# Performance work log

Measured on AMD Instinct MI355X. Metric: run time of the kernel, lower is better.

## Reference

```python
import jax, jax.numpy as jnp
import numpy as np

M, U, H, C, EMB, HID = 4096, 8, 8, 64, 64, 128
N = M * U            # 32768 nodes
E = 131072           # edges
D = H * C            # 512 = heads * hidden_channels
NUM_LAYERS = 4
IN0 = 6              # 2 coords + mask + speed + cost + arrival
SCALE = np.float32(1.0 / np.sqrt(C))

def _lin(x, W, b):
    return x @ W + b

def _transformer_conv(x, src, dst, Wq, bq, Wk, bk, Wv, bv, Ws, bs):
    # PyG TransformerConv: x_j = x[src], x_i = x[dst]; softmax over edges per dst
    n = x.shape[0]
    q = _lin(x, Wq, bq).reshape(n, H, C)
    k = _lin(x, Wk, bk).reshape(n, H, C)
    v = _lin(x, Wv, bv).reshape(n, H, C)
    alpha = jnp.einsum('ehc,ehc->eh', q[dst], k[src]) * SCALE   # [E,H]
    amax = jax.ops.segment_max(alpha, dst, num_segments=n)       # [N,H]
    ex = jnp.exp(alpha - amax[dst])
    denom = jax.ops.segment_sum(ex, dst, num_segments=n)         # [N,H]
    agg = jax.ops.segment_sum(ex[:, :, None] * v[src], dst, num_segments=n)  # [N,H,C]
    out = agg / (denom[:, :, None] + 1e-16)
    return out.reshape(n, D) + _lin(x, Ws, bs)                   # concat heads + root skip

def _forward(mission_coords, uavs_info, speeds, cost_matrix, arrival_times,
             Wq0, bq0, Wk0, bk0, Wv0, bv0, Ws0, bs0,
             Wq, bq, Wk, bk, Wv, bv, Ws, bs,
             fc_W, fc_b, aW1, ab1, aW2, ab2, cW1, cb1, cW2, cb2,
             edge_index, batch, action_mask):
    mc = jnp.broadcast_to(mission_coords[:, None, :], (M, U, 2))
    mk = jnp.broadcast_to(action_mask[:, None, None].astype(jnp.float32), (M, U, 1))
    sp = jnp.broadcast_to(speeds[None, :, None], (M, U, 1))
    cm = cost_matrix.T[:, :, None]
    at = arrival_times.T[:, :, None]
    x = jnp.concatenate([mc, mk, sp, cm, at], axis=-1).reshape(N, IN0)
    src, dst = edge_index[0], edge_index[1]
    x = jax.nn.relu(_transformer_conv(x, src, dst, Wq0, bq0, Wk0, bk0, Wv0, bv0, Ws0, bs0))
    for l in range(NUM_LAYERS - 1):
        x = jax.nn.relu(_transformer_conv(x, src, dst, Wq[l], bq[l], Wk[l], bk[l], Wv[l], bv[l], Ws[l], bs[l]))
    new_batch = jnp.repeat(batch, U)                             # [N]
    sums = jax.ops.segment_sum(x, new_batch, num_segments=1)
    cnts = jax.ops.segment_sum(jnp.ones((N,), x.dtype), new_batch, num_segments=1)
    pooled = sums / cnts[:, None]                                # [1, D]
    emb = _lin(pooled, fc_W, fc_b)                               # [1, EMB]
    emb_exp = jnp.tile(emb, (U, 1))                              # [U, EMB]
    combined = jnp.concatenate([uavs_info, emb_exp, speeds[:, None]], axis=-1)  # [U, EMB+3]
    action_probs = jax.nn.softmax(_lin(jax.nn.relu(_lin(combined, aW1, ab1)), aW2, ab2), axis=-1)
    state_values = _lin(jax.nn.relu(_lin(combined, cW1, cb1)), cW2, cb2)
    return action_probs, state_values

def setup_inputs() -> dict:
    key = jax.random.key(0)
    ks = jax.random.split(key, 40)
    def nrm(i, shape, s=0.05):
        return jax.random.normal(ks[i], shape, jnp.float32) * s
    z = lambda *s: jnp.zeros(s, jnp.float32)
    L = NUM_LAYERS - 1
    inp = dict(
        mission_coords=jax.random.uniform(ks[0], (M, 2), jnp.float32),
        uavs_info=nrm(1, (U, 2), 1.0),
        speeds=jax.random.uniform(ks[2], (U,), jnp.float32) + 0.5,
        cost_matrix=jax.random.uniform(ks[3], (U, M), jnp.float32),
        arrival_times=jax.random.uniform(ks[4], (U, M), jnp.float32),
        edge_index=jax.random.randint(ks[5], (2, E), 0, N),
        batch=jnp.zeros((M,), jnp.int32),
        action_mask=jax.random.randint(ks[6], (M,), 0, 2),
        Wq0=nrm(7, (IN0, D)), bq0=z(D), Wk0=nrm(8, (IN0, D)), bk0=z(D),
        Wv0=nrm(9, (IN0, D)), bv0=z(D), Ws0=nrm(10, (IN0, D)), bs0=z(D),
        Wq=nrm(11, (L, D, D)), bq=z(L, D), Wk=nrm(12, (L, D, D)), bk=z(L, D),
        Wv=nrm(13, (L, D, D)), bv=z(L, D), Ws=nrm(14, (L, D, D)), bs=z(L, D),
        fc_W=nrm(15, (D, EMB)), fc_b=z(EMB),
        aW1=nrm(16, (EMB + 3, HID)), ab1=z(HID), aW2=nrm(17, (HID, M)), ab2=z(M),
        cW1=nrm(18, (EMB + 3, HID)), cb1=z(HID), cW2=nrm(19, (HID, 1)), cb2=z(1),
    )
    return inp

def reference(mission_coords, edge_index, batch, uavs_info, action_mask, speeds,
              cost_matrix, arrival_times,
              Wq0, bq0, Wk0, bk0, Wv0, bv0, Ws0, bs0,
              Wq, bq, Wk, bk, Wv, bv, Ws, bs,
              fc_W, fc_b, aW1, ab1, aW2, ab2, cW1, cb1, cW2, cb2):
    return _forward(mission_coords, uavs_info, speeds, cost_matrix, arrival_times,
                    Wq0, bq0, Wk0, bk0, Wv0, bv0, Ws0, bs0,
                    Wq, bq, Wk, bk, Wv, bv, Ws, bs,
                    fc_W, fc_b, aW1, ab1, aW2, ab2, cW1, cb1, cW2, cb2,
                    edge_index, batch, action_mask)
```

## Files before the change

kernel.cpp:

```cpp
#include <hip/hip_runtime.h>
#include <stdint.h>

typedef unsigned char u8;
typedef unsigned short u16;
typedef unsigned long long u64;
typedef __attribute__((ext_vector_type(8))) unsigned short u16x8;
typedef __attribute__((ext_vector_type(8))) __bf16 bf16x8;
typedef __attribute__((ext_vector_type(4))) float f32x4;
typedef __attribute__((ext_vector_type(2))) float f32x2;

#define NNODES 32768
#define NEDGES 131072
#define DDIM 512
#define QK4 2048
#define MM 4096
#define UU 8


__device__ __forceinline__ u16 f2bf(float f) {
    unsigned u = __builtin_bit_cast(unsigned, f);
    u += 0x7FFFu + ((u >> 16) & 1u);
    return (u16)(u >> 16);
}
__device__ __forceinline__ float bf2f(u16 h) {
    return __builtin_bit_cast(float, (unsigned)h << 16);
}
__device__ __forceinline__ void enc8(const float* f, int* lo, int* hi) {
    int a = __builtin_amdgcn_cvt_pk_fp8_f32(f[0], f[1], 0, false);
    a = __builtin_amdgcn_cvt_pk_fp8_f32(f[2], f[3], a, true);
    int b = __builtin_amdgcn_cvt_pk_fp8_f32(f[4], f[5], 0, false);
    b = __builtin_amdgcn_cvt_pk_fp8_f32(f[6], f[7], b, true);
    *lo = a;
    *hi = b;
}
__device__ __forceinline__ void dec8(int lo, int hi, float* f) {
    f32x2 a = __builtin_amdgcn_cvt_pk_f32_fp8(lo, false);
    f32x2 b = __builtin_amdgcn_cvt_pk_f32_fp8(lo, true);
    f32x2 c = __builtin_amdgcn_cvt_pk_f32_fp8(hi, false);
    f32x2 d = __builtin_amdgcn_cvt_pk_f32_fp8(hi, true);
    f[0] = a[0]; f[1] = a[1]; f[2] = b[0]; f[3] = b[1];
    f[4] = c[0]; f[5] = c[1]; f[6] = d[0]; f[7] = d[1];
}

__device__ __forceinline__ void load_lds16(const void* g, void* l) {
    __builtin_amdgcn_global_load_lds((__attribute__((address_space(1))) unsigned int*)(void*)g,
                                     (__attribute__((address_space(3))) unsigned int*)l, 16, 0, 0);
}

__global__ void k_prep(const float* __restrict__ mc, const int* __restrict__ mask,
                       const float* __restrict__ sp, const float* __restrict__ cm,
                       const float* __restrict__ at, float* __restrict__ x0,
                       const float* __restrict__ bq, const float* __restrict__ bk,
                       const float* __restrict__ bv, const float* __restrict__ bs,
                       float* __restrict__ bcat,
                       int* __restrict__ deg, float* __restrict__ pooled) {
    int b = blockIdx.x;
    int t = threadIdx.x;
    if (b < 128) {
        int node = b * 256 + t;
        deg[node] = 0;
        int m = node >> 3, u = node & 7;
        float* o = x0 + (size_t)node * 6;
        o[0] = mc[m * 2];
        o[1] = mc[m * 2 + 1];
        o[2] = (float)mask[m];
        o[3] = sp[u];
        o[4] = cm[u * MM + m];
        o[5] = at[u * MM + m];
    } else if (b < 152) {
        int i = (b - 128) * 256 + t;
        int n = i & (QK4 - 1);
        int l = i >> 11;
        int ty = n >> 9, nn = n & 511;
        const float* p = (ty == 0) ? bq : (ty == 1) ? bk : (ty == 2) ? bv : bs;
        bcat[(size_t)l * QK4 + n] = p[l * DDIM + nn];
    } else {
        pooled[(b - 152) * 256 + t] = 0.f;
    }
}

__global__ void k_c0(const float* __restrict__ Wq0, const float* __restrict__ bq0,
                     const float* __restrict__ Wk0, const float* __restrict__ bk0,
                     float* __restrict__ C0) {
    int i = threadIdx.x;
    if (i >= 392) return;
    int h = i / 49, r = i % 49;
    int d0 = h * 64;
    float s = 0.f;
    if (r < 36) {
        int a = r / 6, b = r % 6;
        for (int d = 0; d < 64; d++) s += Wq0[a * DDIM + d0 + d] * Wk0[b * DDIM + d0 + d];
    } else if (r < 42) {
        int a = r - 36;
        for (int d = 0; d < 64; d++) s += Wq0[a * DDIM + d0 + d] * bk0[d0 + d];
    } else if (r < 48) {
        int b = r - 42;
        for (int d = 0; d < 64; d++) s += Wk0[b * DDIM + d0 + d] * bq0[d0 + d];
    } else {
        for (int d = 0; d < 64; d++) s += bq0[d0 + d] * bk0[d0 + d];
    }
    C0[i] = s;
}

__global__ void k_wt(const float* __restrict__ Wq, const float* __restrict__ Wk,
                     const float* __restrict__ Wv, const float* __restrict__ Ws,
                     u16* __restrict__ Wt) {
    __shared__ float tile[32][33];
    int q = blockIdx.z;
    int l = q >> 2, t = q & 3;
    const float* src = ((t == 0) ? Wq : (t == 1) ? Wk : (t == 2) ? Wv : Ws) + (size_t)l * DDIM * DDIM;
    int k0 = blockIdx.x * 32, n0 = blockIdx.y * 32;
    int tx = threadIdx.x, ty = threadIdx.y;
#pragma unroll
    for (int r = 0; r < 4; r++) tile[ty + 8 * r][tx] = src[(size_t)(k0 + ty + 8 * r) * DDIM + n0 + tx];
    __syncthreads();
    u16* dst = Wt + (size_t)l * QK4 * DDIM + (size_t)t * DDIM * DDIM;
#pragma unroll
    for (int r = 0; r < 4; r++) {
        int n = n0 + ty + 8 * r;
        dst[(size_t)n * DDIM + k0 + tx] = f2bf(tile[tx][ty + 8 * r]);
    }
}

__global__ void k_count(const int* __restrict__ dst, int* __restrict__ deg) {
    int e = blockIdx.x * 256 + threadIdx.x;
    if (e < NEDGES) atomicAdd(&deg[dst[e]], 1);
}

__global__ __launch_bounds__(1024) void k_scan(const int* __restrict__ deg, int* __restrict__ offs,
                                               int* __restrict__ cursor) {
    __shared__ int sums[1024];
    int t = threadIdx.x;
    int base = t * 32;
    int local[32];
    int s = 0;
#pragma unroll
    for (int i = 0; i < 32; i++) { local[i] = s; s += deg[base + i]; }
    sums[t] = s;
    __syncthreads();
    for (int d = 1; d < 1024; d <<= 1) {
        int v = (t >= d) ? sums[t - d] : 0;
        __syncthreads();
        sums[t] += v;
        __syncthreads();
    }
    int excl = (t == 0) ? 0 : sums[t - 1];
#pragma unroll
    for (int i = 0; i < 32; i++) {
        int o = excl + local[i];
        offs[base + i] = o;
        cursor[base + i] = o;
    }
    if (t == 1023) offs[NNODES] = sums[1023];
}

__global__ void k_scatter(const int* __restrict__ src, const int* __restrict__ dst,
                          int* __restrict__ cursor, int* __restrict__ ssrc) {
    int e = blockIdx.x * 256 + threadIdx.x;
    if (e < NEDGES) {
        int pos = atomicAdd(&cursor[dst[e]], 1);
        ssrc[pos] = src[e];
    }
}

__global__ __launch_bounds__(256) void k_attn0(const float* __restrict__ x0, const float* __restrict__ C0,
                                               const float* __restrict__ Wv0, const float* __restrict__ bv0,
                                               const float* __restrict__ Ws0, const float* __restrict__ bs0,
                                               const int* __restrict__ offs, const int* __restrict__ ssrc,
                                               u16* __restrict__ Xout) {
    const int lane = threadIdx.x & 63;
    const int wv = threadIdx.x >> 6;
    const int h = lane & 7;
    float wV[8][6], wS[8][6], bV[8], bS[8];
#pragma unroll
    for (int j = 0; j < 8; ++j) {
        int c = lane + 64 * j;
        bV[j] = bv0[c];
        bS[j] = bs0[c];
#pragma unroll
        for (int a = 0; a < 6; ++a) {
            wV[j][a] = Wv0[a * DDIM + c];
            wS[j][a] = Ws0[a * DDIM + c];
        }
    }
    float Ah[36], uh[6], wh[6], ch;
#pragma unroll
    for (int r = 0; r < 36; ++r) Ah[r] = C0[h * 49 + r];
#pragma unroll
    for (int a = 0; a < 6; ++a) uh[a] = C0[h * 49 + 36 + a];
#pragma unroll
    for (int a = 0; a < 6; ++a) wh[a] = C0[h * 49 + 42 + a];
    ch = C0[h * 49 + 48];

    int node0 = (blockIdx.x * 4 + wv) * 8;
    for (int nn = 0; nn < 8; ++nn) {
        int node = node0 + nn;
        float xi[6];
#pragma unroll
        for (int a = 0; a < 6; ++a) xi[a] = x0[(size_t)node * 6 + a];
        float m = -INFINITY, l = 0.f;
        float xh[6];
#pragma unroll
        for (int a = 0; a < 6; ++a) xh[a] = 0.f;
        const int e0 = offs[node], e1 = offs[node + 1];
        for (int e = e0; e < e1; ++e) {
            int s = ssrc[e];
            float xj[6];
#pragma unroll
            for (int a = 0; a < 6; ++a) xj[a] = x0[(size_t)s * 6 + a];
            float alpha = ch;
#pragma unroll
            for (int a = 0; a < 6; ++a) {
                float t = uh[a];
#pragma unroll
                for (int b = 0; b < 6; ++b) t += Ah[a * 6 + b] * xj[b];
                alpha += xi[a] * t;
            }
#pragma unroll
            for (int b = 0; b < 6; ++b) alpha += wh[b] * xj[b];
            alpha *= 0.125f;
            float nm = fmaxf(m, alpha);
            float corr = __expf(m - nm);
            float p = __expf(alpha - nm);
            l = l * corr + p;
#pragma unroll
            for (int a = 0; a < 6; ++a) xh[a] = xh[a] * corr + p * xj[a];
            m = nm;
        }
#pragma unroll
        for (int j = 0; j < 8; ++j) {
            float lb = __shfl(l, j, 64);
            float num = lb * bV[j];
#pragma unroll
            for (int a = 0; a < 6; ++a) num += __shfl(xh[a], j, 64) * wV[j][a];
            float skip = bS[j];
#pragma unroll
            for (int a = 0; a < 6; ++a) skip += xi[a] * wS[j][a];
            float r = num / (lb + 1e-16f) + skip;
            Xout[(size_t)node * DDIM + lane + 64 * j] = f2bf(fmaxf(r, 0.f));
        }
    }
}

__global__ __launch_bounds__(256, 4) void k_gemm(const u16* __restrict__ X, const u16* __restrict__ Wt,
                                                 const float* __restrict__ bcat, u8* __restrict__ Q8,
                                                 u8* __restrict__ KV8, u16* __restrict__ S16) {
    __shared__ __align__(16) u16 smem[2 * 128 * 64];
    u16* As = smem;
    u16* Bs = smem + 128 * 64;
    const int tid = threadIdx.x;
    const int lane = tid & 63;
    const int w = tid >> 6;
    const int wm = w & 1, wn = w >> 1;
    const int bid = blockIdx.x;
    const int xcd = bid & 7;
    const int s = bid >> 3;
    const size_t arow0 = (size_t)(xcd * 32 + (s >> 4)) * 128;
    const size_t brow0 = (size_t)(s & 15) * 128;
    const int bt = (int)(brow0 >> 7);

    f32x4 acc[4][4];
#pragma unroll
    for (int i = 0; i < 4; i++)
#pragma unroll
        for (int j = 0; j < 4; j++) acc[i][j] = (f32x4){0.f, 0.f, 0.f, 0.f};

    const int la = lane & 7;
    const int quad = lane >> 4;
    const int lm = lane & 15;

    for (int kt = 0; kt < 8; ++kt) {
        const int k0 = kt * 64;
#pragma unroll
        for (int t = 0; t < 4; ++t) {
            int idx = (w * 4 + t) * 64 + lane;
            int m = idx >> 3;
            int c = la ^ (m & 7);
            const u16* ga = X + (arow0 + m) * DDIM + (k0 + c * 8);
            const u16* gb = Wt + (brow0 + m) * DDIM + (k0 + c * 8);
            load_lds16(ga, &As[(size_t)((w * 4 + t) * 64) * 8]);
            load_lds16(gb, &Bs[(size_t)((w * 4 + t) * 64) * 8]);
        }
        __syncthreads();
#pragma unroll
        for (int kk = 0; kk < 2; ++kk) {
            bf16x8 af[4], bfg[4];
            int c = kk * 4 + quad;
#pragma unroll
            for (int i = 0; i < 4; ++i) {
                int m = wm * 64 + i * 16 + lm;
                int slot = m * 8 + (c ^ (m & 7));
                af[i] = *(const bf16x8*)&As[(size_t)slot * 8];
            }
#pragma unroll
            for (int j = 0; j < 4; ++j) {
                int n = wn * 64 + j * 16 + lm;
                int slot = n * 8 + (c ^ (n & 7));
                bfg[j] = *(const bf16x8*)&Bs[(size_t)slot * 8];
            }
#pragma unroll
            for (int i = 0; i < 4; ++i)
#pragma unroll
                for (int j = 0; j < 4; ++j)
                    acc[i][j] = __builtin_amdgcn_mfma_f32_16x16x32_bf16(af[i], bfg[j], acc[i][j], 0, 0, 0);
        }
        __syncthreads();
    }

    float biasv[4];
#pragma unroll
    for (int j = 0; j < 4; ++j) biasv[j] = bcat[brow0 + wn * 64 + j * 16 + lm];

    u16* stg = smem;
    const int chunk = lane & 7;
    const int rrow = lane >> 3;
    const int colbase = (int)brow0 + wn * 64 + chunk * 8;
#pragma unroll
    for (int p = 0; p < 2; ++p) {
        __syncthreads();
#pragma unroll
        for (int ii = 0; ii < 2; ++ii) {
            int i = p * 2 + ii;
#pragma unroll
            for (int j = 0; j < 4; ++j) {
#pragma unroll
                for (int r = 0; r < 4; ++r) {
                    int lr = ii * 16 + quad * 4 + r;
                    int lc = j * 16 + lm;
                    stg[(size_t)(w * 32 + lr) * 72 + lc] = f2bf(acc[i][j][r] + biasv[j]);
                }
            }
        }
        __syncthreads();
#pragma unroll
        for (int it = 0; it < 4; ++it) {
            int row = it * 8 + rrow;
            u16x8 v = *(const u16x8*)&stg[(size_t)(w * 32 + row) * 72 + chunk * 8];
            size_t grow = arow0 + wm * 64 + p * 32 + row;
            if (bt < 4) {
                float f[8];
#pragma unroll
                for (int j = 0; j < 8; j++) f[j] = bf2f(v[j]);
                int lo, hi;
                enc8(f, &lo, &hi);
                *(int2*)(Q8 + grow * 512 + colbase) = make_int2(lo, hi);
            } else if (bt < 12) {
                float f[8];
#pragma unroll
                for (int j = 0; j < 8; j++) f[j] = bf2f(v[j]);
                int lo, hi;
                enc8(f, &lo, &hi);
                int kvcol = (bt < 8) ? (colbase - 512) : (colbase - 1024);
                int ofs = (bt < 8) ? 0 : 8;
                *(int2*)(KV8 + grow * 1024 + (size_t)(kvcol >> 3) * 16 + ofs) = make_int2(lo, hi);
            } else {
                *(u16x8*)(S16 + grow * 512 + (colbase - 1536)) = v;
            }
        }
    }
}

__global__ __launch_bounds__(256) void k_attn(const u8* __restrict__ Q8, const u8* __restrict__ KV8,
                                              const u16* __restrict__ S16, const int* __restrict__ offs,
                                              const int* __restrict__ ssrc, u16* __restrict__ Xout) {
    const int lane = threadIdx.x & 63;
    const int node = blockIdx.x * 4 + (threadIdx.x >> 6);
    const u64 q8 = *(const u64*)(Q8 + (size_t)node * 512 + (size_t)lane * 8);
    float qf[8];
    dec8((int)(q8 & 0xFFFFFFFFull), (int)(q8 >> 32), qf);
    float m = -INFINITY, l = 0.f;
    float acc[8];
#pragma unroll
    for (int j = 0; j < 8; j++) acc[j] = 0.f;
    const int e0 = offs[node], e1 = offs[node + 1];
    int e = e0;
    while (e < e1) {
        int nb = e1 - e;
        if (nb > 4) nb = 4;
        int4 kvb[4];
#pragma unroll
        for (int i = 0; i < 4; ++i) {
            if (i < nb) {
                int s = ssrc[e + i];
                kvb[i] = *(const int4*)(KV8 + (size_t)s * 1024 + (size_t)lane * 16);
            }
        }
#pragma unroll
        for (int i = 0; i < 4; ++i) {
            if (i >= nb) break;
            int4 kv = kvb[i];
            f32x2 k01 = __builtin_amdgcn_cvt_pk_f32_fp8(kv.x, false);
            f32x2 k23 = __builtin_amdgcn_cvt_pk_f32_fp8(kv.x, true);
            f32x2 k45 = __builtin_amdgcn_cvt_pk_f32_fp8(kv.y, false);
            f32x2 k67 = __builtin_amdgcn_cvt_pk_f32_fp8(kv.y, true);
            float d = qf[0] * k01[0] + qf[1] * k01[1] + qf[2] * k23[0] + qf[3] * k23[1] +
                      qf[4] * k45[0] + qf[5] * k45[1] + qf[6] * k67[0] + qf[7] * k67[1];
            d += __shfl_xor(d, 1, 64);
            d += __shfl_xor(d, 2, 64);
            d += __shfl_xor(d, 4, 64);
            float a = d * 0.125f;
            float nm = fmaxf(m, a);
            float corr = __expf(m - nm);
            float p = __expf(a - nm);
            l = l * corr + p;
            f32x2 v01 = __builtin_amdgcn_cvt_pk_f32_fp8(kv.z, false);
            f32x2 v23 = __builtin_amdgcn_cvt_pk_f32_fp8(kv.z, true);
            f32x2 v45 = __builtin_amdgcn_cvt_pk_f32_fp8(kv.w, false);
            f32x2 v67 = __builtin_amdgcn_cvt_pk_f32_fp8(kv.w, true);
            acc[0] = acc[0] * corr + p * v01[0];
            acc[1] = acc[1] * corr + p * v01[1];
            acc[2] = acc[2] * corr + p * v23[0];
            acc[3] = acc[3] * corr + p * v23[1];
            acc[4] = acc[4] * corr + p * v45[0];
            acc[5] = acc[5] * corr + p * v45[1];
            acc[6] = acc[6] * corr + p * v67[0];
            acc[7] = acc[7] * corr + p * v67[1];
            m = nm;
        }
        e += nb;
    }
    float inv = 1.0f / (l + 1e-16f);
    const u16x8 sv = *(const u16x8*)(S16 + (size_t)node * 512 + (size_t)lane * 8);
    u16x8 o;
#pragma unroll
    for (int j = 0; j < 8; j++) {
        float r = acc[j] * inv + bf2f(sv[j]);
        o[j] = f2bf(fmaxf(r, 0.f));
    }
    *(u16x8*)(Xout + (size_t)node * DDIM + (size_t)lane * 8) = o;
}

__global__ __launch_bounds__(256) void k_pool(const u16* __restrict__ X, float* __restrict__ pooled) {
    __shared__ float red[4][64][8];
    int t = threadIdx.x;
    int chunk = t & 63;
    int rofs = t >> 6;
    float s[8];
#pragma unroll
    for (int j = 0; j < 8; j++) s[j] = 0.f;
    int nd0 = blockIdx.x * 256;
    for (int nd = nd0 + rofs; nd < nd0 + 256; nd += 4) {
        u16x8 v = *(const u16x8*)&X[(size_t)nd * DDIM + chunk * 8];
#pragma unroll
        for (int j = 0; j < 8; j++) s[j] += bf2f(v[j]);
    }
#pragma unroll
    for (int j = 0; j < 8; j++) red[rofs][chunk][j] = s[j];
    __syncthreads();
    if (t < 64) {
#pragma unroll
        for (int j = 0; j < 8; j++) {
            float o = red[0][t][j] + red[1][t][j] + red[2][t][j] + red[3][t][j];
            atomicAdd(&pooled[t * 8 + j], o);
        }
    }
}

__global__ __launch_bounds__(1024) void k_heads(const float* __restrict__ pooled, const float* __restrict__ fcW,
                                                const float* __restrict__ fcb, const float* __restrict__ ui,
                                                const float* __restrict__ sp, const float* __restrict__ aW1,
                                                const float* __restrict__ ab1, const float* __restrict__ cW1,
                                                const float* __restrict__ cb1, const float* __restrict__ cW2,
                                                const float* __restrict__ cb2, float* __restrict__ hidden_a,
                                                float* __restrict__ out) {
    __shared__ float spool[512];
    __shared__ float semb[64];
    __shared__ float shc[8][128];
    int t = threadIdx.x;
    if (t < 512) spool[t] = pooled[t] * (1.0f / 32768.0f);
    __syncthreads();
    if (t < 64) {
        float s = fcb[t];
        for (int k = 0; k < 512; k++) s += spool[k] * fcW[k * 64 + t];
        semb[t] = s;
    }
    __syncthreads();
    int u = t >> 7, j = t & 127;
    float u0 = ui[u * 2], u1 = ui[u * 2 + 1], uspd = sp[u];
    float ha = ab1[j] + u0 * aW1[j] + u1 * aW1[128 + j] + uspd * aW1[66 * 128 + j];
    float hc = cb1[j] + u0 * cW1[j] + u1 * cW1[128 + j] + uspd * cW1[66 * 128 + j];
    for (int k = 0; k < 64; k++) {
        float e = semb[k];
        ha += e * aW1[(2 + k) * 128 + j];
        hc += e * cW1[(2 + k) * 128 + j];
    }
    ha = fmaxf(ha, 0.f);
    hc = fmaxf(hc, 0.f);
    hidden_a[u * 128 + j] = ha;
    shc[u][j] = hc;
    __syncthreads();
    if (t < 8) {
        float s = cb2[0];
        for (int k = 0; k < 128; k++) s += shc[t][k] * cW2[k];
        out[NNODES + t] = s;
    }
}

__global__ __launch_bounds__(1024) void k_actor(const float* __restrict__ hidden_a, const float* __restrict__ aW2,
                                                const float* __restrict__ ab2, float* __restrict__ out) {
    __shared__ float h[128];
    __shared__ float red[1024];
    int u = blockIdx.x, t = threadIdx.x;
    if (t < 128) h[t] = hidden_a[u * 128 + t];
    __syncthreads();
    float lg[4];
#pragma unroll
    for (int p = 0; p < 4; p++) {
        int mcol = t + p * 1024;
        float s = ab2[mcol];
        for (int k = 0; k < 128; k++) s += h[k] * aW2[(size_t)k * MM + mcol];
        lg[p] = s;
    }
    float mx = fmaxf(fmaxf(lg[0], lg[1]), fmaxf(lg[2], lg[3]));
    red[t] = mx;
    __syncthreads();
    for (int s2 = 512; s2 > 0; s2 >>= 1) {
        if (t < s2) red[t] = fmaxf(red[t], red[t + s2]);
        __syncthreads();
    }
    mx = red[0];
    __syncthreads();
    float e[4], sum = 0.f;
#pragma unroll
    for (int p = 0; p < 4; p++) {
        e[p] = __expf(lg[p] - mx);
        sum += e[p];
    }
    red[t] = sum;
    __syncthreads();
    for (int s2 = 512; s2 > 0; s2 >>= 1) {
        if (t < s2) red[t] += red[t + s2];
        __syncthreads();
    }
    float inv = 1.0f / red[0];
#pragma unroll
    for (int p = 0; p < 4; p++) out[(size_t)u * MM + t + p * 1024] = e[p] * inv;
}

extern "C" void kernel_launch(void* const* d_in, const int* in_sizes, int n_in,
                              void* d_out, int out_size, void* d_ws, size_t ws_size,
                              hipStream_t stream) {
    const float* mc   = (const float*)d_in[0];
    const float* ui   = (const float*)d_in[1];
    const float* sp   = (const float*)d_in[2];
    const float* cm   = (const float*)d_in[3];
    const float* at   = (const float*)d_in[4];
    const int*   eidx = (const int*)d_in[5];
    const int*   mask = (const int*)d_in[7];
    const float* Wq0 = (const float*)d_in[8];
    const float* bq0 = (const float*)d_in[9];
    const float* Wk0 = (const float*)d_in[10];
    const float* bk0 = (const float*)d_in[11];
    const float* Wv0 = (const float*)d_in[12];
    const float* bv0 = (const float*)d_in[13];
    const float* Ws0 = (const float*)d_in[14];
    const float* bs0 = (const float*)d_in[15];
    const float* Wq = (const float*)d_in[16];
    const float* bq = (const float*)d_in[17];
    const float* Wk = (const float*)d_in[18];
    const float* bk = (const float*)d_in[19];
    const float* Wv = (const float*)d_in[20];
    const float* bv = (const float*)d_in[21];
    const float* Ws = (const float*)d_in[22];
    const float* bs = (const float*)d_in[23];
    const float* fcW = (const float*)d_in[24];
    const float* fcb = (const float*)d_in[25];
    const float* aW1 = (const float*)d_in[26];
    const float* ab1 = (const float*)d_in[27];
    const float* aW2 = (const float*)d_in[28];
    const float* ab2 = (const float*)d_in[29];
    const float* cW1 = (const float*)d_in[30];
    const float* cb1 = (const float*)d_in[31];
    const float* cW2 = (const float*)d_in[32];
    const float* cb2 = (const float*)d_in[33];
    float* out = (float*)d_out;

    const int* esrc = eidx;
    const int* edst = eidx + NEDGES;

    char* ws = (char*)d_ws;
    size_t off = 0;
    auto alloc = [&](size_t bytes) -> void* {
        void* p = ws + off;
        off += (bytes + 255) & ~(size_t)255;
        return p;
    };
    u8*    Q8    = (u8*)alloc((size_t)NNODES * 512);
    u8*    KV8   = (u8*)alloc((size_t)NNODES * 1024);
    u16*   S16   = (u16*)alloc((size_t)NNODES * 512 * 2);
    u16*   X     = (u16*)alloc((size_t)NNODES * DDIM * 2);
    u16*   Wt    = (u16*)alloc((size_t)3 * QK4 * DDIM * 2);
    float* bcat  = (float*)alloc((size_t)3 * QK4 * 4);
    float* C0    = (float*)alloc((size_t)392 * 4);
    float* x0    = (float*)alloc((size_t)NNODES * 6 * 4);
    int*   deg   = (int*)alloc((size_t)NNODES * 4);
    int*   offs  = (int*)alloc((size_t)(NNODES + 1) * 4);
    int*   cursor= (int*)alloc((size_t)NNODES * 4);
    int*   ssrc  = (int*)alloc((size_t)NEDGES * 4);
    float* pooled= (float*)alloc((size_t)512 * 4);
    float* hidden_a = (float*)alloc((size_t)UU * 128 * 4);
    (void)ws_size; (void)in_sizes; (void)n_in; (void)out_size;

    k_prep<<<154, 256, 0, stream>>>(mc, mask, sp, cm, at, x0, bq, bk, bv, bs, bcat, deg, pooled);
    k_c0<<<1, 512, 0, stream>>>(Wq0, bq0, Wk0, bk0, C0);
    {
        dim3 g(16, 16, 12), b(32, 8);
        k_wt<<<g, b, 0, stream>>>(Wq, Wk, Wv, Ws, Wt);
    }
    k_count<<<NEDGES / 256, 256, 0, stream>>>(edst, deg);
    k_scan<<<1, 1024, 0, stream>>>(deg, offs, cursor);
    k_scatter<<<NEDGES / 256, 256, 0, stream>>>(esrc, edst, cursor, ssrc);

    k_attn0<<<1024, 256, 0, stream>>>(x0, C0, Wv0, bv0, Ws0, bs0, offs, ssrc, X);

    for (int l = 0; l < 3; ++l) {
        k_gemm<<<4096, 256, 0, stream>>>(X, Wt + (size_t)l * QK4 * DDIM, bcat + (size_t)l * QK4, Q8, KV8, S16);
        k_attn<<<NNODES / 4, 256, 0, stream>>>(Q8, KV8, S16, offs, ssrc, X);
    }

    k_pool<<<128, 256, 0, stream>>>(X, pooled);
    k_heads<<<1, 1024, 0, stream>>>(pooled, fcW, fcb, ui, sp, aW1, ab1, cW1, cb1, cW2, cb2, hidden_a, out);
    k_actor<<<UU, 1024, 0, stream>>>(hidden_a, aW2, ab2, out);
}
```

Measured before the change: 622.7 us.

## Process two destination nodes per wavefront in attention and raise gemm occupancy hint

The attention kernel now has each wavefront handle two adjacent destination nodes, interleaving their edge gathers so up to eight KV loads are in flight per iteration. The grid is halved to match. This aims to raise memory-level parallelism on the irregular gathers, at the cost of more registers per wave and fewer waves overall. Separately, the gemm kernel's launch-bounds occupancy hint goes from 4 to 5 blocks per CU, which may force register spilling.

```diff
diff --git a/kernel.cpp b/kernel.cpp
--- a/kernel.cpp
+++ b/kernel.cpp
@@ -242,7 +242,7 @@
     }
 }
 
-__global__ __launch_bounds__(256, 4) void k_gemm(const u16* __restrict__ X, const u16* __restrict__ Wt,
+__global__ __launch_bounds__(256, 5) void k_gemm(const u16* __restrict__ X, const u16* __restrict__ Wt,
                                                  const float* __restrict__ bcat, u8* __restrict__ Q8,
                                                  u8* __restrict__ KV8, u16* __restrict__ S16) {
     __shared__ __align__(16) u16 smem[2 * 128 * 64];
@@ -364,70 +364,111 @@
                                               const u16* __restrict__ S16, const int* __restrict__ offs,
                                               const int* __restrict__ ssrc, u16* __restrict__ Xout) {
     const int lane = threadIdx.x & 63;
-    const int node = blockIdx.x * 4 + (threadIdx.x >> 6);
-    const u64 q8 = *(const u64*)(Q8 + (size_t)node * 512 + (size_t)lane * 8);
-    float qf[8];
-    dec8((int)(q8 & 0xFFFFFFFFull), (int)(q8 >> 32), qf);
-    float m = -INFINITY, l = 0.f;
-    float acc[8];
-#pragma unroll
-    for (int j = 0; j < 8; j++) acc[j] = 0.f;
-    const int e0 = offs[node], e1 = offs[node + 1];
-    int e = e0;
-    while (e < e1) {
-        int nb = e1 - e;
-        if (nb > 4) nb = 4;
-        int4 kvb[4];
+    const int w = threadIdx.x >> 6;
+    const int nodeA = (blockIdx.x * 4 + w) * 2;
+    const int nodeB = nodeA + 1;
+    const u64 q8a = *(const u64*)(Q8 + (size_t)nodeA * 512 + (size_t)lane * 8);
+    const u64 q8b = *(const u64*)(Q8 + (size_t)nodeB * 512 + (size_t)lane * 8);
+    float qA[8], qB[8];
+    dec8((int)(q8a & 0xFFFFFFFFull), (int)(q8a >> 32), qA);
+    dec8((int)(q8b & 0xFFFFFFFFull), (int)(q8b >> 32), qB);
+    float mA = -INFINITY, lA = 0.f, mB = -INFINITY, lB = 0.f;
+    float accA[8], accB[8];
+#pragma unroll
+    for (int j = 0; j < 8; j++) { accA[j] = 0.f; accB[j] = 0.f; }
+    int eA = offs[nodeA];
+    const int e1A = offs[nodeA + 1];
+    int eB = e1A;
+    const int e1B = offs[nodeB + 1];
+    while (eA < e1A || eB < e1B) {
+        int nbA = e1A - eA; if (nbA > 4) nbA = 4; if (nbA < 0) nbA = 0;
+        int nbB = e1B - eB; if (nbB > 4) nbB = 4; if (nbB < 0) nbB = 0;
+        int4 ka[4], kb[4];
+#pragma unroll
+        for (int i = 0; i < 4; ++i)
+            if (i < nbA) ka[i] = *(const int4*)(KV8 + (size_t)ssrc[eA + i] * 1024 + (size_t)lane * 16);
+#pragma unroll
+        for (int i = 0; i < 4; ++i)
+            if (i < nbB) kb[i] = *(const int4*)(KV8 + (size_t)ssrc[eB + i] * 1024 + (size_t)lane * 16);
 #pragma unroll
         for (int i = 0; i < 4; ++i) {
-            if (i < nb) {
-                int s = ssrc[e + i];
-                kvb[i] = *(const int4*)(KV8 + (size_t)s * 1024 + (size_t)lane * 16);
-            }
-        }
-#pragma unroll
-        for (int i = 0; i < 4; ++i) {
-            if (i >= nb) break;
-            int4 kv = kvb[i];
+            if (i >= nbA) break;
+            int4 kv = ka[i];
             f32x2 k01 = __builtin_amdgcn_cvt_pk_f32_fp8(kv.x, false);
             f32x2 k23 = __builtin_amdgcn_cvt_pk_f32_fp8(kv.x, true);
             f32x2 k45 = __builtin_amdgcn_cvt_pk_f32_fp8(kv.y, false);
             f32x2 k67 = __builtin_amdgcn_cvt_pk_f32_fp8(kv.y, true);
-            float d = qf[0] * k01[0] + qf[1] * k01[1] + qf[2] * k23[0] + qf[3] * k23[1] +
-                      qf[4] * k45[0] + qf[5] * k45[1] + qf[6] * k67[0] + qf[7] * k67[1];
+            float d = qA[0] * k01[0] + qA[1] * k01[1] + qA[2] * k23[0] + qA[3] * k23[1] +
+                      qA[4] * k45[0] + qA[5] * k45[1] + qA[6] * k67[0] + qA[7] * k67[1];
             d += __shfl_xor(d, 1, 64);
             d += __shfl_xor(d, 2, 64);
             d += __shfl_xor(d, 4, 64);
             float a = d * 0.125f;
-            float nm = fmaxf(m, a);
-            float corr = __expf(m - nm);
+            float nm = fmaxf(mA, a);
+            float corr = __expf(mA - nm);
             float p = __expf(a - nm);
-            l = l * corr + p;
+            lA = lA * corr + p;
             f32x2 v01 = __builtin_amdgcn_cvt_pk_f32_fp8(kv.z, false);
             f32x2 v23 = __builtin_amdgcn_cvt_pk_f32_fp8(kv.z, true);
             f32x2 v45 = __builtin_amdgcn_cvt_pk_f32_fp8(kv.w, false);
             f32x2 v67 = __builtin_amdgcn_cvt_pk_f32_fp8(kv.w, true);
-            acc[0] = acc[0] * corr + p * v01[0];
-            acc[1] = acc[1] * corr + p * v01[1];
-            acc[2] = acc[2] * corr + p * v23[0];
-            acc[3] = acc[3] * corr + p * v23[1];
-            acc[4] = acc[4] * corr + p * v45[0];
-            acc[5] = acc[5] * corr + p * v45[1];
-            acc[6] = acc[6] * corr + p * v67[0];
-            acc[7] = acc[7] * corr + p * v67[1];
-            m = nm;
-        }
-        e += nb;
-    }
-    float inv = 1.0f / (l + 1e-16f);
-    const u16x8 sv = *(const u16x8*)(S16 + (size_t)node * 512 + (size_t)lane * 8);
-    u16x8 o;
+            accA[0] = accA[0] * corr + p * v01[0];
+            accA[1] = accA[1] * corr + p * v01[1];
+            accA[2] = accA[2] * corr + p * v23[0];
+            accA[3] = accA[3] * corr + p * v23[1];
+            accA[4] = accA[4] * corr + p * v45[0];
+            accA[5] = accA[5] * corr + p * v45[1];
+            accA[6] = accA[6] * corr + p * v67[0];
+            accA[7] = accA[7] * corr + p * v67[1];
+            mA = nm;
+        }
+#pragma unroll
+        for (int i = 0; i < 4; ++i) {
+            if (i >= nbB) break;
+            int4 kv = kb[i];
+            f32x2 k01 = __builtin_amdgcn_cvt_pk_f32_fp8(kv.x, false);
+            f32x2 k23 = __builtin_amdgcn_cvt_pk_f32_fp8(kv.x, true);
+            f32x2 k45 = __builtin_amdgcn_cvt_pk_f32_fp8(kv.y, false);
+            f32x2 k67 = __builtin_amdgcn_cvt_pk_f32_fp8(kv.y, true);
+            float d = qB[0] * k01[0] + qB[1] * k01[1] + qB[2] * k23[0] + qB[3] * k23[1] +
+                      qB[4] * k45[0] + qB[5] * k45[1] + qB[6] * k67[0] + qB[7] * k67[1];
+            d += __shfl_xor(d, 1, 64);
+            d += __shfl_xor(d, 2, 64);
+            d += __shfl_xor(d, 4, 64);
+            float a = d * 0.125f;
+            float nm = fmaxf(mB, a);
+            float corr = __expf(mB - nm);
+            float p = __expf(a - nm);
+            lB = lB * corr + p;
+            f32x2 v01 = __builtin_amdgcn_cvt_pk_f32_fp8(kv.z, false);
+            f32x2 v23 = __builtin_amdgcn_cvt_pk_f32_fp8(kv.z, true);
+            f32x2 v45 = __builtin_amdgcn_cvt_pk_f32_fp8(kv.w, false);
+            f32x2 v67 = __builtin_amdgcn_cvt_pk_f32_fp8(kv.w, true);
+            accB[0] = accB[0] * corr + p * v01[0];
+            accB[1] = accB[1] * corr + p * v01[1];
+            accB[2] = accB[2] * corr + p * v23[0];
+            accB[3] = accB[3] * corr + p * v23[1];
+            accB[4] = accB[4] * corr + p * v45[0];
+            accB[5] = accB[5] * corr + p * v45[1];
+            accB[6] = accB[6] * corr + p * v67[0];
+            accB[7] = accB[7] * corr + p * v67[1];
+            mB = nm;
+        }
+        eA += nbA;
+        eB += nbB;
+    }
+    const u16x8 svA = *(const u16x8*)(S16 + (size_t)nodeA * 512 + (size_t)lane * 8);
+    const u16x8 svB = *(const u16x8*)(S16 + (size_t)nodeB * 512 + (size_t)lane * 8);
+    float invA = 1.0f / (lA + 1e-16f);
+    float invB = 1.0f / (lB + 1e-16f);
+    u16x8 oA, oB;
 #pragma unroll
     for (int j = 0; j < 8; j++) {
-        float r = acc[j] * inv + bf2f(sv[j]);
-        o[j] = f2bf(fmaxf(r, 0.f));
-    }
-    *(u16x8*)(Xout + (size_t)node * DDIM + (size_t)lane * 8) = o;
+        oA[j] = f2bf(fmaxf(accA[j] * invA + bf2f(svA[j]), 0.f));
+        oB[j] = f2bf(fmaxf(accB[j] * invB + bf2f(svB[j]), 0.f));
+    }
+    *(u16x8*)(Xout + (size_t)nodeA * DDIM + (size_t)lane * 8) = oA;
+    *(u16x8*)(Xout + (size_t)nodeB * DDIM + (size_t)lane * 8) = oB;
 }
 
 __global__ __launch_bounds__(256) void k_pool(const u16* __restrict__ X, float* __restrict__ pooled) {
@@ -615,7 +656,7 @@
 
     for (int l = 0; l < 3; ++l) {
         k_gemm<<<4096, 256, 0, stream>>>(X, Wt + (size_t)l * QK4 * DDIM, bcat + (size_t)l * QK4, Q8, KV8, S16);
-        k_attn<<<NNODES / 4, 256, 0, stream>>>(Q8, KV8, S16, offs, ssrc, X);
+        k_attn<<<4096, 256, 0, stream>>>(Q8, KV8, S16, offs, ssrc, X);
     }
 
     k_pool<<<128, 256, 0, stream>>>(X, pooled);
```

Result: slower. 955.1 us (+53.4%).

## Permute QKV weight columns to emit interleaved KV directly; prefetch next edge in attention

Applied to the files above, without the earlier changes.

Reorders the K and V columns of the concatenated weight and bias so the GEMM output is already in the interleaved per-8 K/V layout. The epilogue store then becomes a plain contiguous write with no remapping. The attention loop replaces batched 4-edge gathers with a single-edge software prefetch of the next KV row. This simplifies control flow but issues fewer concurrent gathers per node.

```diff
diff --git a/kernel.cpp b/kernel.cpp
--- a/kernel.cpp
+++ b/kernel.cpp
@@ -71,9 +71,15 @@
         int i = (b - 128) * 256 + t;
         int n = i & (QK4 - 1);
         int l = i >> 11;
-        int ty = n >> 9, nn = n & 511;
-        const float* p = (ty == 0) ? bq : (ty == 1) ? bk : (ty == 2) ? bv : bs;
-        bcat[(size_t)l * QK4 + n] = p[l * DDIM + nn];
+        const float* p;
+        int col;
+        if (n < 512) { p = bq; col = n; }
+        else if (n < 1536) {
+            int g = n - 512, c = g >> 4, r = g & 15;
+            if (r < 8) { p = bk; col = c * 8 + r; }
+            else { p = bv; col = c * 8 + r - 8; }
+        } else { p = bs; col = n - 1536; }
+        bcat[(size_t)l * QK4 + n] = p[l * DDIM + col];
     } else {
         pooled[(b - 152) * 256 + t] = 0.f;
     }
@@ -114,10 +120,15 @@
 #pragma unroll
     for (int r = 0; r < 4; r++) tile[ty + 8 * r][tx] = src[(size_t)(k0 + ty + 8 * r) * DDIM + n0 + tx];
     __syncthreads();
-    u16* dst = Wt + (size_t)l * QK4 * DDIM + (size_t)t * DDIM * DDIM;
+    u16* dst = Wt + (size_t)l * QK4 * DDIM;
 #pragma unroll
     for (int r = 0; r < 4; r++) {
-        int n = n0 + ty + 8 * r;
+        int nn = n0 + ty + 8 * r;
+        int n;
+        if (t == 0) n = nn;
+        else if (t == 1) n = 512 + ((nn >> 3) << 4) + (nn & 7);
+        else if (t == 2) n = 512 + ((nn >> 3) << 4) + 8 + (nn & 7);
+        else n = 1536 + nn;
         dst[(size_t)n * DDIM + k0 + tx] = f2bf(tile[tx][ty + 8 * r]);
     }
 }
@@ -350,9 +361,7 @@
                 for (int j = 0; j < 8; j++) f[j] = bf2f(v[j]);
                 int lo, hi;
                 enc8(f, &lo, &hi);
-                int kvcol = (bt < 8) ? (colbase - 512) : (colbase - 1024);
-                int ofs = (bt < 8) ? 0 : 8;
-                *(int2*)(KV8 + grow * 1024 + (size_t)(kvcol >> 3) * 16 + ofs) = make_int2(lo, hi);
+                *(int2*)(KV8 + grow * 1024 + (colbase - 512)) = make_int2(lo, hi);
             } else {
                 *(u16x8*)(S16 + grow * 512 + (colbase - 1536)) = v;
             }
@@ -373,51 +382,38 @@
 #pragma unroll
     for (int j = 0; j < 8; j++) acc[j] = 0.f;
     const int e0 = offs[node], e1 = offs[node + 1];
-    int e = e0;
-    while (e < e1) {
-        int nb = e1 - e;
-        if (nb > 4) nb = 4;
-        int4 kvb[4];
-#pragma unroll
-        for (int i = 0; i < 4; ++i) {
-            if (i < nb) {
-                int s = ssrc[e + i];
-                kvb[i] = *(const int4*)(KV8 + (size_t)s * 1024 + (size_t)lane * 16);
-            }
-        }
-#pragma unroll
-        for (int i = 0; i < 4; ++i) {
-            if (i >= nb) break;
-            int4 kv = kvb[i];
-            f32x2 k01 = __builtin_amdgcn_cvt_pk_f32_fp8(kv.x, false);
-            f32x2 k23 = __builtin_amdgcn_cvt_pk_f32_fp8(kv.x, true);
-            f32x2 k45 = __builtin_amdgcn_cvt_pk_f32_fp8(kv.y, false);
-            f32x2 k67 = __builtin_amdgcn_cvt_pk_f32_fp8(kv.y, true);
-            float d = qf[0] * k01[0] + qf[1] * k01[1] + qf[2] * k23[0] + qf[3] * k23[1] +
-                      qf[4] * k45[0] + qf[5] * k45[1] + qf[6] * k67[0] + qf[7] * k67[1];
-            d += __shfl_xor(d, 1, 64);
-            d += __shfl_xor(d, 2, 64);
-            d += __shfl_xor(d, 4, 64);
-            float a = d * 0.125f;
-            float nm = fmaxf(m, a);
-            float corr = __expf(m - nm);
-            float p = __expf(a - nm);
-            l = l * corr + p;
-            f32x2 v01 = __builtin_amdgcn_cvt_pk_f32_fp8(kv.z, false);
-            f32x2 v23 = __builtin_amdgcn_cvt_pk_f32_fp8(kv.z, true);
-            f32x2 v45 = __builtin_amdgcn_cvt_pk_f32_fp8(kv.w, false);
-            f32x2 v67 = __builtin_amdgcn_cvt_pk_f32_fp8(kv.w, true);
-            acc[0] = acc[0] * corr + p * v01[0];
-            acc[1] = acc[1] * corr + p * v01[1];
-            acc[2] = acc[2] * corr + p * v23[0];
-            acc[3] = acc[3] * corr + p * v23[1];
-            acc[4] = acc[4] * corr + p * v45[0];
-            acc[5] = acc[5] * corr + p * v45[1];
-            acc[6] = acc[6] * corr + p * v67[0];
-            acc[7] = acc[7] * corr + p * v67[1];
-            m = nm;
-        }
-        e += nb;
+    int4 kvn;
+    if (e0 < e1) kvn = *(const int4*)(KV8 + (size_t)ssrc[e0] * 1024 + (size_t)lane * 16);
+    for (int e = e0; e < e1; ++e) {
+        int4 kv = kvn;
+        if (e + 1 < e1) kvn = *(const int4*)(KV8 + (size_t)ssrc[e + 1] * 1024 + (size_t)lane * 16);
+        f32x2 k01 = __builtin_amdgcn_cvt_pk_f32_fp8(kv.x, false);
+        f32x2 k23 = __builtin_amdgcn_cvt_pk_f32_fp8(kv.x, true);
+        f32x2 k45 = __builtin_amdgcn_cvt_pk_f32_fp8(kv.y, false);
+        f32x2 k67 = __builtin_amdgcn_cvt_pk_f32_fp8(kv.y, true);
+        float d = qf[0] * k01[0] + qf[1] * k01[1] + qf[2] * k23[0] + qf[3] * k23[1] +
+                  qf[4] * k45[0] + qf[5] * k45[1] + qf[6] * k67[0] + qf[7] * k67[1];
+        d += __shfl_xor(d, 1, 64);
+        d += __shfl_xor(d, 2, 64);
+        d += __shfl_xor(d, 4, 64);
+        float a = d * 0.125f;
+        float nm = fmaxf(m, a);
+        float corr = __expf(m - nm);
+        float p = __expf(a - nm);
+        l = l * corr + p;
+        f32x2 v01 = __builtin_amdgcn_cvt_pk_f32_fp8(kv.z, false);
+        f32x2 v23 = __builtin_amdgcn_cvt_pk_f32_fp8(kv.z, true);
+        f32x2 v45 = __builtin_amdgcn_cvt_pk_f32_fp8(kv.w, false);
+        f32x2 v67 = __builtin_amdgcn_cvt_pk_f32_fp8(kv.w, true);
+        acc[0] = acc[0] * corr + p * v01[0];
+        acc[1] = acc[1] * corr + p * v01[1];
+        acc[2] = acc[2] * corr + p * v23[0];
+        acc[3] = acc[3] * corr + p * v23[1];
+        acc[4] = acc[4] * corr + p * v45[0];
+        acc[5] = acc[5] * corr + p * v45[1];
+        acc[6] = acc[6] * corr + p * v67[0];
+        acc[7] = acc[7] * corr + p * v67[1];
+        m = nm;
     }
     float inv = 1.0f / (l + 1e-16f);
     const u16x8 sv = *(const u16x8*)(S16 + (size_t)node * 512 + (size_t)lane * 8);
```

Result: slower. 639.2 us (+2.6%).
